# Kernel optimization log

Hardware: AMD Instinct MI355X
Metric: run time of the kernel (lower is better)

## Reference

```python
import jax, jax.numpy as jnp
import numpy as np

D_MODEL = 256
NUM_HEADS = 8
HEAD_DIM = D_MODEL // NUM_HEADS
SCALE = HEAD_DIM ** -0.5
LN_EPS = 1e-5


def setup_inputs() -> dict:
    key = jax.random.key(0)
    ks = jax.random.split(key, 16)
    B, N, H, W = 1, 8, 16, 16
    s = 1.0 / np.sqrt(D_MODEL)
    inp = {
        'features': jax.random.normal(ks[0], (B, N, H, W, D_MODEL), jnp.float32),
        'pointmaps': jax.random.normal(ks[1], (B, N, H, W, 3), jnp.float32),
        'Wq': jax.random.normal(ks[2], (D_MODEL, D_MODEL), jnp.float32) * s,
        'bq': jnp.zeros((D_MODEL,), jnp.float32),
        'Wk': jax.random.normal(ks[3], (D_MODEL, D_MODEL), jnp.float32) * s,
        'bk': jnp.zeros((D_MODEL,), jnp.float32),
        'Wv': jax.random.normal(ks[4], (D_MODEL, D_MODEL), jnp.float32) * s,
        'bv': jnp.zeros((D_MODEL,), jnp.float32),
        'Wo': jax.random.normal(ks[5], (D_MODEL, D_MODEL), jnp.float32) * s,
        'bo': jnp.zeros((D_MODEL,), jnp.float32),
        'beta': jnp.asarray(1.0, jnp.float32),
        'k_w1': jax.random.normal(ks[6], (32, 1), jnp.float32) * 0.1,
        'k_b1': jnp.zeros((32,), jnp.float32),
        'k_w2': jax.random.normal(ks[7], (1, 32), jnp.float32) * 0.1,
        'k_b2': jnp.full((1,), -1.0, jnp.float32),
        'ln_g': jnp.ones((D_MODEL,), jnp.float32),
        'ln_b': jnp.zeros((D_MODEL,), jnp.float32),
    }
    return inp


def _gasa_forward(features, pointmaps, Wq, bq, Wk, bk, Wv, bv, Wo, bo,
                  beta, k_w1, k_b1, k_w2, k_b2, ln_g, ln_b):
    B, N, H, W, D = features.shape
    L = N * H * W
    x = features.reshape(B, L, D)

    # QKV projections (torch Linear: x @ W.T + b)
    Q = (x @ Wq.T + bq).reshape(B, L, NUM_HEADS, HEAD_DIM).transpose(0, 2, 1, 3)
    K = (x @ Wk.T + bk).reshape(B, L, NUM_HEADS, HEAD_DIM).transpose(0, 2, 1, 3)
    V = (x @ Wv.T + bv).reshape(B, L, NUM_HEADS, HEAD_DIM).transpose(0, 2, 1, 3)

    # semantic scores [B, h, L, L]
    scores = jnp.einsum('bhqd,bhkd->bhqk', Q, K) * SCALE

    # geometric bias: pairwise 3D distances + tiny MLP kernel, clamp to [-10, 0]
    pts = pointmaps.reshape(B, L, 3)
    diff = pts[:, :, None, :] - pts[:, None, :, :]           # [B, L, L, 3]
    sq = jnp.sum(diff * diff, axis=-1)                        # [B, L, L]
    dist = jnp.where(sq > 0, jnp.sqrt(jnp.where(sq > 0, sq, 1.0)), 0.0)
    h = jax.nn.relu(dist[..., None] * k_w1[:, 0] + k_b1)      # [B, L, L, 32]
    bias = h @ k_w2[0] + k_b2[0]                              # [B, L, L]
    bias = jnp.clip(bias, -10.0, 0.0)

    scores = scores + beta * bias[:, None, :, :]
    probs = jax.nn.softmax(scores, axis=-1)
    out = jnp.einsum('bhqk,bhkd->bhqd', probs, V)
    out = out.transpose(0, 2, 1, 3).reshape(B, L, D)
    out = out @ Wo.T + bo

    # residual + LayerNorm
    y = x + out
    mu = jnp.mean(y, axis=-1, keepdims=True)
    var = jnp.mean(jnp.square(y - mu), axis=-1, keepdims=True)
    y = (y - mu) * jax.lax.rsqrt(var + LN_EPS) * ln_g + ln_b
    return y.reshape(B, N, H, W, D)


def reference(features, pointmaps, Wq, bq, Wk, bk, Wv, bv, Wo, bo,
              beta, k_w1, k_b1, k_w2, k_b2, ln_g, ln_b):
    return _gasa_forward(features, pointmaps, Wq, bq, Wk, bk, Wv, bv, Wo, bo,
                         beta, k_w1, k_b1, k_w2, k_b2, ln_g, ln_b)
```

## Files before the change

kernel.cpp:

```cpp
#include <hip/hip_runtime.h>
#include <math.h>

#define L_SEQ 2048
#define DM    256
#define NH    8
#define HD    32

typedef __attribute__((ext_vector_type(8))) short bf16x8;
typedef __attribute__((ext_vector_type(4))) float f32x4;

__device__ __forceinline__ unsigned short f2bf(float f) {
    unsigned int u = __builtin_bit_cast(unsigned int, f);
    u += 0x7fff + ((u >> 16) & 1);
    return (unsigned short)(u >> 16);
}

__global__ __launch_bounds__(256) void cvt_inputs(
    const float* __restrict__ x, const float* __restrict__ wq,
    const float* __restrict__ wk, const float* __restrict__ wv,
    const float* __restrict__ wo,
    unsigned short* __restrict__ xb, unsigned short* __restrict__ wqb,
    unsigned short* __restrict__ wkb, unsigned short* __restrict__ wvb,
    unsigned short* __restrict__ wob)
{
    int e = (blockIdx.x * 256 + threadIdx.x) * 4;
    const float* src; unsigned short* dst; int off;
    if      (e < 524288) { src = x;  dst = xb;  off = e; }
    else if (e < 589824) { src = wq; dst = wqb; off = e - 524288; }
    else if (e < 655360) { src = wk; dst = wkb; off = e - 589824; }
    else if (e < 720896) { src = wv; dst = wvb; off = e - 655360; }
    else                 { src = wo; dst = wob; off = e - 720896; }
    float4 v = *(const float4*)(src + off);
    ushort4 o; o.x = f2bf(v.x); o.y = f2bf(v.y); o.z = f2bf(v.z); o.w = f2bf(v.w);
    *(ushort4*)(dst + off) = o;
}

__global__ __launch_bounds__(256) void gemm_qkv(
    const unsigned short* __restrict__ xb,
    const unsigned short* __restrict__ wqb, const float* __restrict__ bq,
    const unsigned short* __restrict__ wkb, const float* __restrict__ bk,
    const unsigned short* __restrict__ wvb, const float* __restrict__ bv,
    unsigned short* __restrict__ Qb, unsigned short* __restrict__ Kb,
    unsigned short* __restrict__ Vb)
{
    const unsigned short* Wm; const float* bias; unsigned short* out;
    if (blockIdx.z == 0)      { Wm = wqb; bias = bq; out = Qb; }
    else if (blockIdx.z == 1) { Wm = wkb; bias = bk; out = Kb; }
    else                      { Wm = wvb; bias = bv; out = Vb; }

    const int t = threadIdx.x, w = t >> 6, lane = t & 63, quad = lane >> 4, c = lane & 15;
    const int r0 = blockIdx.x * 16;
    const int c0 = w * 64;

    f32x4 acc[4] = {};
    for (int kt = 0; kt < 8; ++kt) {
        bf16x8 a = *(const bf16x8*)(xb + (size_t)(r0 + c) * DM + kt * 32 + quad * 8);
#pragma unroll
        for (int ct = 0; ct < 4; ++ct) {
            bf16x8 b = *(const bf16x8*)(Wm + (size_t)(c0 + ct * 16 + c) * DM + kt * 32 + quad * 8);
            acc[ct] = __builtin_amdgcn_mfma_f32_16x16x32_bf16(a, b, acc[ct], 0, 0, 0);
        }
    }
#pragma unroll
    for (int ct = 0; ct < 4; ++ct) {
        float bc = bias[c0 + ct * 16 + c];
#pragma unroll
        for (int reg = 0; reg < 4; ++reg) {
            int r = r0 + quad * 4 + reg;
            out[(size_t)r * DM + c0 + ct * 16 + c] = f2bf(acc[ct][reg] + bc);
        }
    }
}

__global__ __launch_bounds__(256) void bias_mlp(
    const float* __restrict__ pts,
    const float* __restrict__ k_w1, const float* __restrict__ k_b1,
    const float* __restrict__ k_w2, const float* __restrict__ k_b2,
    const float* __restrict__ beta_p,
    unsigned short* __restrict__ biasP)
{
    const int i  = blockIdx.y;
    const int p0 = (blockIdx.x * 256 + threadIdx.x) * 4;
    const float xi = pts[i * 3], yi = pts[i * 3 + 1], zi = pts[i * 3 + 2];
    const float beta = beta_p[0], b2 = k_b2[0];

    float dist[4];
#pragma unroll
    for (int v = 0; v < 4; ++v) {
        int p = p0 + v, loc = p & 31, base = p & ~31;
        int k = base + (loc >> 1) + 16 * (loc & 1);
        float dx = xi - pts[k * 3], dy = yi - pts[k * 3 + 1], dz = zi - pts[k * 3 + 2];
        dist[v] = sqrtf(dx * dx + dy * dy + dz * dz);
    }
    float s[4] = {0.f, 0.f, 0.f, 0.f};
#pragma unroll
    for (int n = 0; n < 32; ++n) {
        float w1 = k_w1[n], b1 = k_b1[n], w2 = k_w2[n];
#pragma unroll
        for (int v = 0; v < 4; ++v) s[v] += fmaxf(fmaf(dist[v], w1, b1), 0.f) * w2;
    }
    ushort4 o; unsigned short* po = (unsigned short*)&o;
#pragma unroll
    for (int v = 0; v < 4; ++v)
        po[v] = f2bf(fminf(fmaxf(s[v] + b2, -10.f), 0.f) * beta);
    *(ushort4*)(biasP + (size_t)i * L_SEQ + p0) = o;
}

__global__ __launch_bounds__(256) void vt_trans(
    const unsigned short* __restrict__ Vb, unsigned short* __restrict__ Vt)
{
    __shared__ unsigned short Vs[32][36];
    const int t = threadIdx.x;
    const int k0 = blockIdx.x * 32, h = blockIdx.y;
    {
        int key = t >> 3, dg = t & 7;
        ushort4 v = *(const ushort4*)(Vb + (size_t)(k0 + key) * DM + h * HD + dg * 4);
        *(ushort4*)&Vs[key][dg * 4] = v;
    }
    __syncthreads();
    {
        int d = t >> 3, cg = t & 7;
        int c0 = cg * 2;
        ushort4 o;
        o.x = Vs[c0][d];      o.y = Vs[c0 + 16][d];
        o.z = Vs[c0 + 1][d];  o.w = Vs[c0 + 17][d];
        *(ushort4*)(Vt + (size_t)(h * HD + d) * L_SEQ + k0 + cg * 4) = o;
    }
}

__global__ __launch_bounds__(256) void attn_mfma(
    const unsigned short* __restrict__ Qb, const unsigned short* __restrict__ Kb,
    const unsigned short* __restrict__ Vt, const unsigned short* __restrict__ biasP,
    unsigned short* __restrict__ Ab)
{
    __shared__ unsigned short Plds[4][32][40];
    __shared__ float Ol[4][32][36];
    __shared__ float Ll[4][32];
    const int t = threadIdx.x, w = t >> 6, lane = t & 63, quad = lane >> 4, c = lane & 15;
    const int h = blockIdx.y, r0 = blockIdx.x * 32;
    const int kbase = w * 512;
    const f32x4 Z = {};

    bf16x8 qf0 = *(const bf16x8*)(Qb + (size_t)(r0 + c) * DM + h * HD + quad * 8);
    bf16x8 qf1 = *(const bf16x8*)(Qb + (size_t)(r0 + 16 + c) * DM + h * HD + quad * 8);

    f32x4 O00 = {}, O01 = {}, O10 = {}, O11 = {};
    float l0[4] = {0.f,0.f,0.f,0.f}, l1[4] = {0.f,0.f,0.f,0.f};

    const float LOG2E = 1.4426950408889634f;
    const float C1 = 0.17677669529663687f * LOG2E;
    const float MC = -10.0f * LOG2E;

    const unsigned short* Kp  = Kb + (size_t)h * HD + quad * 8;
    const unsigned short* Vp0 = Vt + (size_t)(h * HD + c) * L_SEQ + quad * 8;
    const unsigned short* Vp1 = Vt + (size_t)(h * HD + 16 + c) * L_SEQ + quad * 8;
    const int br0 = r0 + quad * 4;

    bf16x8 kf0 = *(const bf16x8*)(Kp + (size_t)(kbase + c) * DM);
    bf16x8 kf1 = *(const bf16x8*)(Kp + (size_t)(kbase + 16 + c) * DM);
    bf16x8 vf0 = *(const bf16x8*)(Vp0 + kbase);
    bf16x8 vf1 = *(const bf16x8*)(Vp1 + kbase);
    unsigned int bu0[4], bu1[4];
#pragma unroll
    for (int reg = 0; reg < 4; ++reg) {
        bu0[reg] = *(const unsigned int*)(biasP + (size_t)(br0 + reg) * L_SEQ + kbase + c * 2);
        bu1[reg] = *(const unsigned int*)(biasP + (size_t)(br0 + 16 + reg) * L_SEQ + kbase + c * 2);
    }

    for (int kt = 0; kt < 16; ++kt) {
        const int kn = kbase + (kt + 1) * 32;
        bf16x8 nk0 = kf0, nk1 = kf1, nv0 = vf0, nv1 = vf1;
        unsigned int nbu0[4], nbu1[4];
#pragma unroll
        for (int reg = 0; reg < 4; ++reg) { nbu0[reg] = bu0[reg]; nbu1[reg] = bu1[reg]; }
        if (kt < 15) {
            nk0 = *(const bf16x8*)(Kp + (size_t)(kn + c) * DM);
            nk1 = *(const bf16x8*)(Kp + (size_t)(kn + 16 + c) * DM);
            nv0 = *(const bf16x8*)(Vp0 + kn);
            nv1 = *(const bf16x8*)(Vp1 + kn);
#pragma unroll
            for (int reg = 0; reg < 4; ++reg) {
                nbu0[reg] = *(const unsigned int*)(biasP + (size_t)(br0 + reg) * L_SEQ + kn + c * 2);
                nbu1[reg] = *(const unsigned int*)(biasP + (size_t)(br0 + 16 + reg) * L_SEQ + kn + c * 2);
            }
        }

        f32x4 S00 = __builtin_amdgcn_mfma_f32_16x16x32_bf16(qf0, kf0, Z, 0, 0, 0);
        f32x4 S01 = __builtin_amdgcn_mfma_f32_16x16x32_bf16(qf0, kf1, Z, 0, 0, 0);
        f32x4 S10 = __builtin_amdgcn_mfma_f32_16x16x32_bf16(qf1, kf0, Z, 0, 0, 0);
        f32x4 S11 = __builtin_amdgcn_mfma_f32_16x16x32_bf16(qf1, kf1, Z, 0, 0, 0);

#pragma unroll
        for (int reg = 0; reg < 4; ++reg) {
            unsigned int u = bu0[reg];
            float blo = __builtin_bit_cast(float, u << 16);
            float bhi = __builtin_bit_cast(float, u & 0xffff0000u);
            float p0 = __builtin_exp2f(fmaf(S00[reg], C1, fmaf(blo, LOG2E, MC)));
            float p1 = __builtin_exp2f(fmaf(S01[reg], C1, fmaf(bhi, LOG2E, MC)));
            l0[reg] += p0 + p1;
            unsigned int pb = (__builtin_bit_cast(unsigned int, p0) >> 16) |
                              (__builtin_bit_cast(unsigned int, p1) & 0xffff0000u);
            *(unsigned int*)&Plds[w][quad * 4 + reg][c * 2] = pb;

            u = bu1[reg];
            blo = __builtin_bit_cast(float, u << 16);
            bhi = __builtin_bit_cast(float, u & 0xffff0000u);
            p0 = __builtin_exp2f(fmaf(S10[reg], C1, fmaf(blo, LOG2E, MC)));
            p1 = __builtin_exp2f(fmaf(S11[reg], C1, fmaf(bhi, LOG2E, MC)));
            l1[reg] += p0 + p1;
            pb = (__builtin_bit_cast(unsigned int, p0) >> 16) |
                 (__builtin_bit_cast(unsigned int, p1) & 0xffff0000u);
            *(unsigned int*)&Plds[w][16 + quad * 4 + reg][c * 2] = pb;
        }

        bf16x8 pa0 = *(const bf16x8*)&Plds[w][c][quad * 8];
        bf16x8 pa1 = *(const bf16x8*)&Plds[w][16 + c][quad * 8];
        O00 = __builtin_amdgcn_mfma_f32_16x16x32_bf16(pa0, vf0, O00, 0, 0, 0);
        O01 = __builtin_amdgcn_mfma_f32_16x16x32_bf16(pa0, vf1, O01, 0, 0, 0);
        O10 = __builtin_amdgcn_mfma_f32_16x16x32_bf16(pa1, vf0, O10, 0, 0, 0);
        O11 = __builtin_amdgcn_mfma_f32_16x16x32_bf16(pa1, vf1, O11, 0, 0, 0);

        kf0 = nk0; kf1 = nk1; vf0 = nv0; vf1 = nv1;
#pragma unroll
        for (int reg = 0; reg < 4; ++reg) { bu0[reg] = nbu0[reg]; bu1[reg] = nbu1[reg]; }
    }

#pragma unroll
    for (int off = 1; off < 16; off <<= 1) {
#pragma unroll
        for (int reg = 0; reg < 4; ++reg) {
            l0[reg] += __shfl_xor(l0[reg], off, 16);
            l1[reg] += __shfl_xor(l1[reg], off, 16);
        }
    }
#pragma unroll
    for (int reg = 0; reg < 4; ++reg) {
        int row = quad * 4 + reg;
        Ol[w][row][c]           = O00[reg];
        Ol[w][row][16 + c]      = O01[reg];
        Ol[w][row + 16][c]      = O10[reg];
        Ol[w][row + 16][16 + c] = O11[reg];
    }
    if (c == 0) {
#pragma unroll
        for (int reg = 0; reg < 4; ++reg) {
            Ll[w][quad * 4 + reg]      = l0[reg];
            Ll[w][quad * 4 + reg + 16] = l1[reg];
        }
    }
    __syncthreads();
    {
        int row = t >> 3, c4 = (t & 7) * 4;
        float4 a = *(const float4*)&Ol[0][row][c4];
        float4 b = *(const float4*)&Ol[1][row][c4];
        float4 d = *(const float4*)&Ol[2][row][c4];
        float4 e = *(const float4*)&Ol[3][row][c4];
        float inv = 1.0f / (Ll[0][row] + Ll[1][row] + Ll[2][row] + Ll[3][row]);
        ushort4 ob;
        ob.x = f2bf((a.x + b.x + d.x + e.x) * inv);
        ob.y = f2bf((a.y + b.y + d.y + e.y) * inv);
        ob.z = f2bf((a.z + b.z + d.z + e.z) * inv);
        ob.w = f2bf((a.w + b.w + d.w + e.w) * inv);
        *(ushort4*)(Ab + (size_t)(r0 + row) * DM + h * HD + c4) = ob;
    }
}

__global__ __launch_bounds__(256) void proj_ln(
    const unsigned short* __restrict__ Ab, const unsigned short* __restrict__ Wob,
    const float* __restrict__ bo, const float* __restrict__ feat,
    const float* __restrict__ ln_g, const float* __restrict__ ln_b,
    float* __restrict__ out)
{
    __shared__ float red1[4][16], red2[4][16];
    const int t = threadIdx.x, w = t >> 6, lane = t & 63, quad = lane >> 4, c = lane & 15;
    const int r0 = blockIdx.x * 16, c0 = w * 64;

    f32x4 acc[4] = {};
    for (int kt = 0; kt < 8; ++kt) {
        bf16x8 a = *(const bf16x8*)(Ab + (size_t)(r0 + c) * DM + kt * 32 + quad * 8);
#pragma unroll
        for (int ct = 0; ct < 4; ++ct) {
            bf16x8 b = *(const bf16x8*)(Wob + (size_t)(c0 + ct * 16 + c) * DM + kt * 32 + quad * 8);
            acc[ct] = __builtin_amdgcn_mfma_f32_16x16x32_bf16(a, b, acc[ct], 0, 0, 0);
        }
    }
    float y[4][4];
    float s1[4] = {0.f,0.f,0.f,0.f}, s2[4] = {0.f,0.f,0.f,0.f};
#pragma unroll
    for (int ct = 0; ct < 4; ++ct) {
        int col = c0 + ct * 16 + c;
        float bc = bo[col];
#pragma unroll
        for (int reg = 0; reg < 4; ++reg) {
            int r = r0 + quad * 4 + reg;
            float v = acc[ct][reg] + bc + feat[(size_t)r * DM + col];
            y[ct][reg] = v;
            s1[reg] += v; s2[reg] += v * v;
        }
    }
#pragma unroll
    for (int off = 1; off < 16; off <<= 1)
#pragma unroll
        for (int reg = 0; reg < 4; ++reg) {
            s1[reg] += __shfl_xor(s1[reg], off, 16);
            s2[reg] += __shfl_xor(s2[reg], off, 16);
        }
    if (c == 0)
#pragma unroll
        for (int reg = 0; reg < 4; ++reg) {
            red1[w][quad * 4 + reg] = s1[reg];
            red2[w][quad * 4 + reg] = s2[reg];
        }
    __syncthreads();
    float mu[4], rs[4];
#pragma unroll
    for (int reg = 0; reg < 4; ++reg) {
        int row = quad * 4 + reg;
        float a1 = red1[0][row] + red1[1][row] + red1[2][row] + red1[3][row];
        float a2 = red2[0][row] + red2[1][row] + red2[2][row] + red2[3][row];
        float m = a1 * (1.0f / 256.0f);
        mu[reg] = m;
        rs[reg] = rsqrtf(a2 * (1.0f / 256.0f) - m * m + 1e-5f);
    }
#pragma unroll
    for (int ct = 0; ct < 4; ++ct) {
        int col = c0 + ct * 16 + c;
        float g = ln_g[col], bb = ln_b[col];
#pragma unroll
        for (int reg = 0; reg < 4; ++reg) {
            int r = r0 + quad * 4 + reg;
            out[(size_t)r * DM + col] = (y[ct][reg] - mu[reg]) * rs[reg] * g + bb;
        }
    }
}

extern "C" void kernel_launch(void* const* d_in, const int* in_sizes, int n_in,
                              void* d_out, int out_size, void* d_ws, size_t ws_size,
                              hipStream_t stream) {
    (void)in_sizes; (void)n_in; (void)out_size; (void)ws_size;
    const float* features  = (const float*)d_in[0];
    const float* pointmaps = (const float*)d_in[1];
    const float* Wq = (const float*)d_in[2];  const float* bq = (const float*)d_in[3];
    const float* Wk = (const float*)d_in[4];  const float* bk = (const float*)d_in[5];
    const float* Wv = (const float*)d_in[6];  const float* bv = (const float*)d_in[7];
    const float* Wo = (const float*)d_in[8];  const float* bo = (const float*)d_in[9];
    const float* beta = (const float*)d_in[10];
    const float* k_w1 = (const float*)d_in[11]; const float* k_b1 = (const float*)d_in[12];
    const float* k_w2 = (const float*)d_in[13]; const float* k_b2 = (const float*)d_in[14];
    const float* ln_g = (const float*)d_in[15]; const float* ln_b = (const float*)d_in[16];
    float* out = (float*)d_out;

    char* W = (char*)d_ws;
    unsigned short* xb    = (unsigned short*)(W);
    unsigned short* Wqb   = (unsigned short*)(W + 1048576);
    unsigned short* Wkb   = (unsigned short*)(W + 1179648);
    unsigned short* Wvb   = (unsigned short*)(W + 1310720);
    unsigned short* Wob   = (unsigned short*)(W + 1441792);
    unsigned short* Qb    = (unsigned short*)(W + 1572864);
    unsigned short* Kb    = (unsigned short*)(W + 2621440);
    unsigned short* Vb    = (unsigned short*)(W + 3670016);
    unsigned short* Vt    = (unsigned short*)(W + 4718592);
    unsigned short* Ab    = (unsigned short*)(W + 5767168);
    unsigned short* biasP = (unsigned short*)(W + 6815744);

    cvt_inputs<<<768, 256, 0, stream>>>(features, Wq, Wk, Wv, Wo, xb, Wqb, Wkb, Wvb, Wob);
    gemm_qkv  <<<dim3(128, 1, 3), 256, 0, stream>>>(xb, Wqb, bq, Wkb, bk, Wvb, bv, Qb, Kb, Vb);
    bias_mlp  <<<dim3(2, 2048),   256, 0, stream>>>(pointmaps, k_w1, k_b1, k_w2, k_b2, beta, biasP);
    vt_trans  <<<dim3(64, 8),     256, 0, stream>>>(Vb, Vt);
    attn_mfma <<<dim3(64, 8),     256, 0, stream>>>(Qb, Kb, Vt, biasP, Ab);
    proj_ln   <<<128,             256, 0, stream>>>(Ab, Wob, bo, features, ln_g, ln_b, out);
}
```

Before: 152.4 us.

## Fuse conversion, QKV GEMM, V transpose and bias MLP into one kernel

Removes the separate fp32-to-bf16 conversion pass by converting inside the GEMM loads with byte permutes (truncating rather than rounding). The QKV projection, V transpose and geometric bias MLP are merged into one launch with block-range dispatch, so V is written directly in transposed layout. proj_ln reads fp32 Wo and converts on the fly. This cuts launches and intermediate buffers, at the cost of truncation rounding and scattered stores for Vt.

```diff
diff --git a/kernel.cpp b/kernel.cpp
--- a/kernel.cpp
+++ b/kernel.cpp
@@ -15,116 +15,104 @@
     return (unsigned short)(u >> 16);
 }
 
-__global__ __launch_bounds__(256) void cvt_inputs(
-    const float* __restrict__ x, const float* __restrict__ wq,
-    const float* __restrict__ wk, const float* __restrict__ wv,
-    const float* __restrict__ wo,
-    unsigned short* __restrict__ xb, unsigned short* __restrict__ wqb,
-    unsigned short* __restrict__ wkb, unsigned short* __restrict__ wvb,
-    unsigned short* __restrict__ wob)
-{
-    int e = (blockIdx.x * 256 + threadIdx.x) * 4;
-    const float* src; unsigned short* dst; int off;
-    if      (e < 524288) { src = x;  dst = xb;  off = e; }
-    else if (e < 589824) { src = wq; dst = wqb; off = e - 524288; }
-    else if (e < 655360) { src = wk; dst = wkb; off = e - 589824; }
-    else if (e < 720896) { src = wv; dst = wvb; off = e - 655360; }
-    else                 { src = wo; dst = wob; off = e - 720896; }
-    float4 v = *(const float4*)(src + off);
-    ushort4 o; o.x = f2bf(v.x); o.y = f2bf(v.y); o.z = f2bf(v.z); o.w = f2bf(v.w);
-    *(ushort4*)(dst + off) = o;
-}
-
-__global__ __launch_bounds__(256) void gemm_qkv(
-    const unsigned short* __restrict__ xb,
-    const unsigned short* __restrict__ wqb, const float* __restrict__ bq,
-    const unsigned short* __restrict__ wkb, const float* __restrict__ bk,
-    const unsigned short* __restrict__ wvb, const float* __restrict__ bv,
-    unsigned short* __restrict__ Qb, unsigned short* __restrict__ Kb,
-    unsigned short* __restrict__ Vb)
-{
-    const unsigned short* Wm; const float* bias; unsigned short* out;
-    if (blockIdx.z == 0)      { Wm = wqb; bias = bq; out = Qb; }
-    else if (blockIdx.z == 1) { Wm = wkb; bias = bk; out = Kb; }
-    else                      { Wm = wvb; bias = bv; out = Vb; }
-
-    const int t = threadIdx.x, w = t >> 6, lane = t & 63, quad = lane >> 4, c = lane & 15;
-    const int r0 = blockIdx.x * 16;
-    const int c0 = w * 64;
-
-    f32x4 acc[4] = {};
-    for (int kt = 0; kt < 8; ++kt) {
-        bf16x8 a = *(const bf16x8*)(xb + (size_t)(r0 + c) * DM + kt * 32 + quad * 8);
-#pragma unroll
-        for (int ct = 0; ct < 4; ++ct) {
-            bf16x8 b = *(const bf16x8*)(Wm + (size_t)(c0 + ct * 16 + c) * DM + kt * 32 + quad * 8);
-            acc[ct] = __builtin_amdgcn_mfma_f32_16x16x32_bf16(a, b, acc[ct], 0, 0, 0);
-        }
-    }
-#pragma unroll
-    for (int ct = 0; ct < 4; ++ct) {
-        float bc = bias[c0 + ct * 16 + c];
-#pragma unroll
-        for (int reg = 0; reg < 4; ++reg) {
-            int r = r0 + quad * 4 + reg;
-            out[(size_t)r * DM + c0 + ct * 16 + c] = f2bf(acc[ct][reg] + bc);
-        }
-    }
-}
-
-__global__ __launch_bounds__(256) void bias_mlp(
-    const float* __restrict__ pts,
+__device__ __forceinline__ bf16x8 ld8_cvt(const float* __restrict__ p) {
+    float4 u = *(const float4*)p;
+    float4 v = *(const float4*)(p + 4);
+    union { unsigned int i[4]; bf16x8 h; } r;
+    r.i[0] = __builtin_amdgcn_perm(__builtin_bit_cast(unsigned int, u.y),
+                                   __builtin_bit_cast(unsigned int, u.x), 0x07060302);
+    r.i[1] = __builtin_amdgcn_perm(__builtin_bit_cast(unsigned int, u.w),
+                                   __builtin_bit_cast(unsigned int, u.z), 0x07060302);
+    r.i[2] = __builtin_amdgcn_perm(__builtin_bit_cast(unsigned int, v.y),
+                                   __builtin_bit_cast(unsigned int, v.x), 0x07060302);
+    r.i[3] = __builtin_amdgcn_perm(__builtin_bit_cast(unsigned int, v.w),
+                                   __builtin_bit_cast(unsigned int, v.z), 0x07060302);
+    return r.h;
+}
+
+__global__ __launch_bounds__(256) void fused_front(
+    const float* __restrict__ x, const float* __restrict__ pts,
+    const float* __restrict__ Wq, const float* __restrict__ bq,
+    const float* __restrict__ Wk, const float* __restrict__ bk,
+    const float* __restrict__ Wv, const float* __restrict__ bv,
     const float* __restrict__ k_w1, const float* __restrict__ k_b1,
     const float* __restrict__ k_w2, const float* __restrict__ k_b2,
     const float* __restrict__ beta_p,
-    unsigned short* __restrict__ biasP)
+    unsigned short* __restrict__ Qb, unsigned short* __restrict__ Kb,
+    unsigned short* __restrict__ Vt, unsigned short* __restrict__ biasP)
 {
-    const int i  = blockIdx.y;
-    const int p0 = (blockIdx.x * 256 + threadIdx.x) * 4;
-    const float xi = pts[i * 3], yi = pts[i * 3 + 1], zi = pts[i * 3 + 2];
-    const float beta = beta_p[0], b2 = k_b2[0];
-
-    float dist[4];
-#pragma unroll
-    for (int v = 0; v < 4; ++v) {
-        int p = p0 + v, loc = p & 31, base = p & ~31;
-        int k = base + (loc >> 1) + 16 * (loc & 1);
-        float dx = xi - pts[k * 3], dy = yi - pts[k * 3 + 1], dz = zi - pts[k * 3 + 2];
-        dist[v] = sqrtf(dx * dx + dy * dy + dz * dz);
-    }
-    float s[4] = {0.f, 0.f, 0.f, 0.f};
-#pragma unroll
-    for (int n = 0; n < 32; ++n) {
-        float w1 = k_w1[n], b1 = k_b1[n], w2 = k_w2[n];
-#pragma unroll
-        for (int v = 0; v < 4; ++v) s[v] += fmaxf(fmaf(dist[v], w1, b1), 0.f) * w2;
-    }
-    ushort4 o; unsigned short* po = (unsigned short*)&o;
-#pragma unroll
-    for (int v = 0; v < 4; ++v)
-        po[v] = f2bf(fminf(fmaxf(s[v] + b2, -10.f), 0.f) * beta);
-    *(ushort4*)(biasP + (size_t)i * L_SEQ + p0) = o;
-}
-
-__global__ __launch_bounds__(256) void vt_trans(
-    const unsigned short* __restrict__ Vb, unsigned short* __restrict__ Vt)
-{
-    __shared__ unsigned short Vs[32][36];
+    const int bx = blockIdx.x;
     const int t = threadIdx.x;
-    const int k0 = blockIdx.x * 32, h = blockIdx.y;
-    {
-        int key = t >> 3, dg = t & 7;
-        ushort4 v = *(const ushort4*)(Vb + (size_t)(k0 + key) * DM + h * HD + dg * 4);
-        *(ushort4*)&Vs[key][dg * 4] = v;
-    }
-    __syncthreads();
-    {
-        int d = t >> 3, cg = t & 7;
-        int c0 = cg * 2;
-        ushort4 o;
-        o.x = Vs[c0][d];      o.y = Vs[c0 + 16][d];
-        o.z = Vs[c0 + 1][d];  o.w = Vs[c0 + 17][d];
-        *(ushort4*)(Vt + (size_t)(h * HD + d) * L_SEQ + k0 + cg * 4) = o;
+
+    if (bx < 384) {
+        const int z  = bx >> 7;
+        const int r0 = (bx & 127) << 4;
+        const int w = t >> 6, lane = t & 63, quad = lane >> 4, c = lane & 15;
+        const int c0 = w * 64;
+        const float* Wm  = (z == 0) ? Wq : (z == 1) ? Wk : Wv;
+        const float* bia = (z == 0) ? bq : (z == 1) ? bk : bv;
+
+        f32x4 acc[4] = {};
+        for (int kt = 0; kt < 8; ++kt) {
+            bf16x8 a = ld8_cvt(x + (size_t)(r0 + c) * DM + kt * 32 + quad * 8);
+#pragma unroll
+            for (int ct = 0; ct < 4; ++ct) {
+                bf16x8 b = ld8_cvt(Wm + (size_t)(c0 + ct * 16 + c) * DM + kt * 32 + quad * 8);
+                acc[ct] = __builtin_amdgcn_mfma_f32_16x16x32_bf16(a, b, acc[ct], 0, 0, 0);
+            }
+        }
+        if (z < 2) {
+            unsigned short* out = (z == 0) ? Qb : Kb;
+#pragma unroll
+            for (int ct = 0; ct < 4; ++ct) {
+                float bc = bia[c0 + ct * 16 + c];
+#pragma unroll
+                for (int reg = 0; reg < 4; ++reg) {
+                    int r = r0 + quad * 4 + reg;
+                    out[(size_t)r * DM + c0 + ct * 16 + c] = f2bf(acc[ct][reg] + bc);
+                }
+            }
+        } else {
+#pragma unroll
+            for (int ct = 0; ct < 4; ++ct) {
+                int col = c0 + ct * 16 + c;
+                float bc = bia[col];
+#pragma unroll
+                for (int reg = 0; reg < 4; ++reg) {
+                    int key = r0 + quad * 4 + reg;
+                    int loc = key & 31;
+                    int pos = (key & ~31) + 2 * (loc & 15) + (loc >> 4);
+                    Vt[(size_t)col * L_SEQ + pos] = f2bf(acc[ct][reg] + bc);
+                }
+            }
+        }
+    } else {
+        const int b = bx - 384;
+        const int i = b >> 1;
+        const int p0 = ((b & 1) * 256 + t) * 4;
+        const float xi = pts[i * 3], yi = pts[i * 3 + 1], zi = pts[i * 3 + 2];
+        const float beta = beta_p[0], b2 = k_b2[0];
+
+        float dist[4];
+#pragma unroll
+        for (int v = 0; v < 4; ++v) {
+            int p = p0 + v, loc = p & 31, base = p & ~31;
+            int k = base + (loc >> 1) + 16 * (loc & 1);
+            float dx = xi - pts[k * 3], dy = yi - pts[k * 3 + 1], dz = zi - pts[k * 3 + 2];
+            dist[v] = sqrtf(dx * dx + dy * dy + dz * dz);
+        }
+        float s[4] = {0.f, 0.f, 0.f, 0.f};
+#pragma unroll
+        for (int n = 0; n < 32; ++n) {
+            float w1 = k_w1[n], b1 = k_b1[n], w2 = k_w2[n];
+#pragma unroll
+            for (int v = 0; v < 4; ++v) s[v] += fmaxf(fmaf(dist[v], w1, b1), 0.f) * w2;
+        }
+        ushort4 o; unsigned short* po = (unsigned short*)&o;
+#pragma unroll
+        for (int v = 0; v < 4; ++v)
+            po[v] = f2bf(fminf(fmaxf(s[v] + b2, -10.f), 0.f) * beta);
+        *(ushort4*)(biasP + (size_t)i * L_SEQ + p0) = o;
     }
 }
 
@@ -198,8 +186,9 @@
             float p0 = __builtin_exp2f(fmaf(S00[reg], C1, fmaf(blo, LOG2E, MC)));
             float p1 = __builtin_exp2f(fmaf(S01[reg], C1, fmaf(bhi, LOG2E, MC)));
             l0[reg] += p0 + p1;
-            unsigned int pb = (__builtin_bit_cast(unsigned int, p0) >> 16) |
-                              (__builtin_bit_cast(unsigned int, p1) & 0xffff0000u);
+            unsigned int pb = __builtin_amdgcn_perm(
+                __builtin_bit_cast(unsigned int, p1),
+                __builtin_bit_cast(unsigned int, p0), 0x07060302);
             *(unsigned int*)&Plds[w][quad * 4 + reg][c * 2] = pb;
 
             u = bu1[reg];
@@ -208,8 +197,9 @@
             p0 = __builtin_exp2f(fmaf(S10[reg], C1, fmaf(blo, LOG2E, MC)));
             p1 = __builtin_exp2f(fmaf(S11[reg], C1, fmaf(bhi, LOG2E, MC)));
             l1[reg] += p0 + p1;
-            pb = (__builtin_bit_cast(unsigned int, p0) >> 16) |
-                 (__builtin_bit_cast(unsigned int, p1) & 0xffff0000u);
+            pb = __builtin_amdgcn_perm(
+                __builtin_bit_cast(unsigned int, p1),
+                __builtin_bit_cast(unsigned int, p0), 0x07060302);
             *(unsigned int*)&Plds[w][16 + quad * 4 + reg][c * 2] = pb;
         }
 
@@ -266,7 +256,7 @@
 }
 
 __global__ __launch_bounds__(256) void proj_ln(
-    const unsigned short* __restrict__ Ab, const unsigned short* __restrict__ Wob,
+    const unsigned short* __restrict__ Ab, const float* __restrict__ Wo,
     const float* __restrict__ bo, const float* __restrict__ feat,
     const float* __restrict__ ln_g, const float* __restrict__ ln_b,
     float* __restrict__ out)
@@ -280,7 +270,7 @@
         bf16x8 a = *(const bf16x8*)(Ab + (size_t)(r0 + c) * DM + kt * 32 + quad * 8);
 #pragma unroll
         for (int ct = 0; ct < 4; ++ct) {
-            bf16x8 b = *(const bf16x8*)(Wob + (size_t)(c0 + ct * 16 + c) * DM + kt * 32 + quad * 8);
+            bf16x8 b = ld8_cvt(Wo + (size_t)(c0 + ct * 16 + c) * DM + kt * 32 + quad * 8);
             acc[ct] = __builtin_amdgcn_mfma_f32_16x16x32_bf16(a, b, acc[ct], 0, 0, 0);
         }
     }
@@ -351,22 +341,16 @@
     float* out = (float*)d_out;
 
     char* W = (char*)d_ws;
-    unsigned short* xb    = (unsigned short*)(W);
-    unsigned short* Wqb   = (unsigned short*)(W + 1048576);
-    unsigned short* Wkb   = (unsigned short*)(W + 1179648);
-    unsigned short* Wvb   = (unsigned short*)(W + 1310720);
-    unsigned short* Wob   = (unsigned short*)(W + 1441792);
-    unsigned short* Qb    = (unsigned short*)(W + 1572864);
-    unsigned short* Kb    = (unsigned short*)(W + 2621440);
-    unsigned short* Vb    = (unsigned short*)(W + 3670016);
-    unsigned short* Vt    = (unsigned short*)(W + 4718592);
-    unsigned short* Ab    = (unsigned short*)(W + 5767168);
-    unsigned short* biasP = (unsigned short*)(W + 6815744);
-
-    cvt_inputs<<<768, 256, 0, stream>>>(features, Wq, Wk, Wv, Wo, xb, Wqb, Wkb, Wvb, Wob);
-    gemm_qkv  <<<dim3(128, 1, 3), 256, 0, stream>>>(xb, Wqb, bq, Wkb, bk, Wvb, bv, Qb, Kb, Vb);
-    bias_mlp  <<<dim3(2, 2048),   256, 0, stream>>>(pointmaps, k_w1, k_b1, k_w2, k_b2, beta, biasP);
-    vt_trans  <<<dim3(64, 8),     256, 0, stream>>>(Vb, Vt);
-    attn_mfma <<<dim3(64, 8),     256, 0, stream>>>(Qb, Kb, Vt, biasP, Ab);
-    proj_ln   <<<128,             256, 0, stream>>>(Ab, Wob, bo, features, ln_g, ln_b, out);
-}
+    unsigned short* Qb    = (unsigned short*)(W);
+    unsigned short* Kb    = (unsigned short*)(W + 1048576);
+    unsigned short* Vt    = (unsigned short*)(W + 2097152);
+    unsigned short* Ab    = (unsigned short*)(W + 3145728);
+    unsigned short* biasP = (unsigned short*)(W + 4194304);
+
+    fused_front<<<4480, 256, 0, stream>>>(features, pointmaps,
+                                          Wq, bq, Wk, bk, Wv, bv,
+                                          k_w1, k_b1, k_w2, k_b2, beta,
+                                          Qb, Kb, Vt, biasP);
+    attn_mfma <<<dim3(64, 8), 256, 0, stream>>>(Qb, Kb, Vt, biasP, Ab);
+    proj_ln   <<<128,         256, 0, stream>>>(Ab, Wo, bo, features, ln_g, ln_b, out);
+}
```

Measured after the change: 151.0 us. No clear change (-0.9%).
